# Kernel tuning notes

Hardware: AMD Instinct MI355X
Metric: run time of the kernel (lower is better)

Reference implementation:

```python
import jax, jax.numpy as jnp
import numpy as np

KROT = 8
DIM = 4096
GROUP = 128
N = 16384  # tokens (batch*seq)


def setup_inputs() -> dict:
    key = jax.random.key(0)
    k1, k2, k3 = jax.random.split(key, 3)
    x = jax.random.normal(k1, (N, DIM), dtype=jnp.float16)
    theta = (jax.random.normal(k2, (KROT, DIM // 2)) * 0.5).astype(jnp.float16)
    # pairs: per rotation layer, a permutation of [0, GROUP) tiled across groups
    # (matches torch.randperm(group_size).repeat(num_groups) in the module).
    rng = np.random.default_rng(0)
    single = np.stack([rng.permutation(GROUP) for _ in range(KROT)]).astype(np.int32)  # (KROT, GROUP)
    pairs = jnp.asarray(np.tile(single, (1, DIM // GROUP)))  # (KROT, DIM)
    channel_scales = jax.random.uniform(k3, (1, DIM), minval=0.5, maxval=1.5).astype(jnp.float16)
    return {"x": x, "pairs": pairs, "theta": theta,
            "channel_scales": channel_scales, "group_size": GROUP}


def reference(x, pairs, theta, channel_scales, group_size):
    """Pairwise Givens rotations + per-channel scaling.

    For each rotation layer k, channels are grouped into blocks of
    `group_size`; consecutive entries (pairs[k, 2i], pairs[k, 2i+1]) within a
    group define a rotated channel pair with angle theta[k, i].
    """
    krot, dim = pairs.shape
    # global channel index = group offset + within-group index from `pairs`
    offs = (jnp.arange(dim) // group_size) * group_size            # (dim,)
    gidx = pairs + offs[None, :]                                   # (krot, dim)
    a_idx = gidx[:, 0::2]                                          # (krot, dim//2)
    b_idx = gidx[:, 1::2]                                          # (krot, dim//2)

    for k in range(krot):  # krot is a small fixed constant (8)
        t = theta[k].astype(jnp.float32)
        c = jnp.cos(t).astype(x.dtype)                             # (dim//2,)
        s = jnp.sin(t).astype(x.dtype)
        xa = x[:, a_idx[k]]                                        # (N, dim//2)
        xb = x[:, b_idx[k]]
        x = x.at[:, a_idx[k]].set(c * xa - s * xb)
        x = x.at[:, b_idx[k]].set(s * xa + c * xb)
    return x * channel_scales
```

## Files before the change

### kernel.cpp

```cpp
#include <hip/hip_runtime.h>
#include <hip/hip_fp16.h>


typedef unsigned int uint32;
typedef unsigned short ushort;

#define DIM    4096
#define GROUP  128
#define KROT   8
#define NGROUP 32
#define TPAD   (GROUP + 1)

typedef float    f32x4 __attribute__((ext_vector_type(4)));
typedef _Float16 f16x8 __attribute__((ext_vector_type(8)));
typedef short    s16x8 __attribute__((ext_vector_type(8)));

__device__ __forceinline__ float bf16_to_f(ushort u) {
    union { uint32 i; float f; } v; v.i = ((uint32)u) << 16; return v.f;
}
__device__ __forceinline__ ushort f_to_bf16(float f) {
    union { float f; uint32 i; } v; v.f = f;
    uint32 x = v.i;
    return (ushort)((x + 0x7fffu + ((x >> 16) & 1u)) >> 16);
}
__device__ __forceinline__ float fp16_to_f(ushort u) {
    __half h = __ushort_as_half(u); return __half2float(h);
}
__device__ __forceinline__ ushort f_to_fp16(float f) {
    return __half_as_ushort(__float2half_rn(f));
}
__device__ __forceinline__ float bcast_f(float x, int lane) {
    return __uint_as_float(__builtin_amdgcn_readlane(__float_as_uint(x), lane));
}

__global__ __launch_bounds__(256) void detect_dtype(const uint32* __restrict__ scw,
                                                    int* __restrict__ flag) {
    __shared__ int cbf[256], cfp16[256];
    int b = 0, h = 0;
    for (int i = threadIdx.x; i < 2048; i += 256) {
        uint32 lo = scw[i] & 0xffffu;
        b += (lo >= 0x3F00u && lo <= 0x3FC0u);
        h += (lo >= 0x3800u && lo <= 0x3E00u);
    }
    cbf[threadIdx.x] = b; cfp16[threadIdx.x] = h;
    __syncthreads();
    for (int s = 128; s > 0; s >>= 1) {
        if (threadIdx.x < s) { cbf[threadIdx.x] += cbf[threadIdx.x + s];
                               cfp16[threadIdx.x] += cfp16[threadIdx.x + s]; }
        __syncthreads();
    }
    if (threadIdx.x == 0)
        *flag = (cbf[0] > 1024) ? 1 : ((cfp16[0] > 1024) ? 2 : 0);
}

__global__ __launch_bounds__(256) void compose_M(
    const int*  __restrict__ pairs,
    const void* __restrict__ thetav,
    const void* __restrict__ scalesv,
    ushort*     __restrict__ Mt,
    const int*  __restrict__ flagp)
{
    __shared__ float tile[64][TPAD];
    const int dt = *flagp;
    if (dt == 0) return;
    const int g    = blockIdx.x >> 1;
    const int half = blockIdx.x & 1;
    const int r0   = half * 64;
    const int tid  = threadIdx.x;
    const int l    = tid & 63;
    const int w    = tid >> 6;
    const int pmine = w * 16 + (l & 15);

    int A[KROT], B[KROT]; float C[KROT], S[KROT];
    #pragma unroll
    for (int k = 0; k < KROT; ++k) {
        A[k] = pairs[k * DIM + g * GROUP + 2 * pmine];
        B[k] = pairs[k * DIM + g * GROUP + 2 * pmine + 1];
        int ti = k * (DIM / 2) + g * (GROUP / 2) + pmine;
        float th = (dt == 1) ? bf16_to_f(((const ushort*)thetav)[ti])
                             : fp16_to_f(((const ushort*)thetav)[ti]);
        float c = __builtin_cosf(th), s = __builtin_sinf(th);
        if (dt == 1) { c = bf16_to_f(f_to_bf16(c)); s = bf16_to_f(f_to_bf16(s)); }
        else         { c = fp16_to_f(f_to_fp16(c)); s = fp16_to_f(f_to_fp16(s)); }
        C[k] = c; S[k] = s;
    }

    for (int idx = tid; idx < 64 * GROUP; idx += 256) {
        int r = idx >> 7, c = idx & 127;
        tile[r][c] = (r0 + r == c) ? 1.0f : 0.0f;
    }
    __syncthreads();

    #pragma unroll
    for (int k = 0; k < KROT; ++k) {
        #pragma unroll
        for (int pp = 0; pp < 16; ++pp) {
            int   a = __builtin_amdgcn_readlane(A[k], pp);
            int   b = __builtin_amdgcn_readlane(B[k], pp);
            float c = bcast_f(C[k], pp);
            float s = bcast_f(S[k], pp);
            float xa = tile[l][a], xb = tile[l][b];
            tile[l][a] = c * xa - s * xb;
            tile[l][b] = s * xa + c * xb;
        }
        __syncthreads();
    }

    for (int it = 0; it < 4; ++it) {
        int idx = it * 256 + tid;
        int j = idx >> 3, cc = idx & 7;
        float sj = (dt == 1) ? bf16_to_f(((const ushort*)scalesv)[g * GROUP + j])
                             : fp16_to_f(((const ushort*)scalesv)[g * GROUP + j]);
        uint32 ws4[4];
        #pragma unroll
        for (int h2 = 0; h2 < 4; ++h2) {
            float lo = tile[cc * 8 + 2 * h2][j]     * sj;
            float hi = tile[cc * 8 + 2 * h2 + 1][j] * sj;
            ushort ulo = (dt == 1) ? f_to_bf16(lo) : f_to_fp16(lo);
            ushort uhi = (dt == 1) ? f_to_bf16(hi) : f_to_fp16(hi);
            ws4[h2] = (uint32)ulo | ((uint32)uhi << 16);
        }
        uint4 v; v.x = ws4[0]; v.y = ws4[1]; v.z = ws4[2]; v.w = ws4[3];
        *(uint4*)(Mt + (size_t)g * GROUP * GROUP + (size_t)j * GROUP
                     + ((size_t)(half * 8 + cc)) * 8) = v;
    }
}

template <int DT>
__device__ __forceinline__ void gemm_core(const ushort* __restrict__ xs,
                                          const ushort* __restrict__ mt,
                                          f32x4 acc[2][4], int l, int wr, int wc)
{
    const int lr = l & 15, q = l >> 4;
    union U { uint4 u; f16x8 h; s16x8 s; };
    #pragma unroll
    for (int kk = 0; kk < 4; ++kk) {
        U av[2];
        #pragma unroll
        for (int mf = 0; mf < 2; ++mf) {
            int r = wr * 32 + mf * 16 + lr;
            int c = (kk * 4 + q) ^ (r & 7);
            av[mf].u = *(const uint4*)(xs + (size_t)r * GROUP + (size_t)c * 8);
        }
        #pragma unroll
        for (int nf = 0; nf < 4; ++nf) {
            int n = wc * 64 + nf * 16 + lr;
            int c = (kk * 4 + q) ^ (n & 7);
            U bv; bv.u = *(const uint4*)(mt + (size_t)n * GROUP + (size_t)c * 8);
            #pragma unroll
            for (int mf = 0; mf < 2; ++mf) {
                if constexpr (DT == 2)
                    acc[mf][nf] = __builtin_amdgcn_mfma_f32_16x16x32_f16(
                        av[mf].h, bv.h, acc[mf][nf], 0, 0, 0);
                else
                    acc[mf][nf] = __builtin_amdgcn_mfma_f32_16x16x32_bf16(
                        av[mf].s, bv.s, acc[mf][nf], 0, 0, 0);
            }
        }
    }
}

__global__ __launch_bounds__(256) void rotate_gemm(
    const void* __restrict__ Xv,
    const ushort* __restrict__ Mt,
    void* __restrict__ Outv,
    const int* __restrict__ flagp,
    const int* __restrict__ pairs,
    const void* __restrict__ thetav,
    const void* __restrict__ scalesv)
{
    __shared__ union __align__(16) {
        struct { ushort xs[64 * GROUP]; ushort mt[GROUP * GROUP]; } s;
        ushort os[64][136];
        struct { float tile[64][TPAD]; float scl[GROUP]; } fb;
    } sh;
    const int dt   = *flagp;
    const int row0 = blockIdx.x * 64;
    const int g    = blockIdx.y;
    const int tid  = threadIdx.x;
    const int l    = tid & 63;
    const int w    = tid >> 6;

    if (dt != 0) {
        const uint4* X4 = (const uint4*)Xv;
        #pragma unroll
        for (int it = 0; it < 4; ++it) {
            int i = it * 256 + tid;
            int r = i >> 4, c = i & 15;
            uint4 v = X4[(size_t)(row0 + r) * (DIM / 8) + g * (GROUP / 8) + c];
            *(uint4*)(sh.s.xs + (size_t)r * GROUP + (size_t)(c ^ (r & 7)) * 8) = v;
        }
        const uint4* M4 = (const uint4*)(Mt + (size_t)g * GROUP * GROUP);
        #pragma unroll
        for (int it = 0; it < 8; ++it) {
            int i = it * 256 + tid;
            int n = i >> 4, c = i & 15;
            uint4 v = M4[i];
            *(uint4*)(sh.s.mt + (size_t)n * GROUP + (size_t)(c ^ (n & 7)) * 8) = v;
        }
        __syncthreads();

        const int wr = w >> 1, wc = w & 1;
        f32x4 acc[2][4];
        #pragma unroll
        for (int mf = 0; mf < 2; ++mf)
            #pragma unroll
            for (int nf = 0; nf < 4; ++nf)
                acc[mf][nf] = (f32x4)0.0f;

        if (dt == 2) gemm_core<2>(sh.s.xs, sh.s.mt, acc, l, wr, wc);
        else         gemm_core<1>(sh.s.xs, sh.s.mt, acc, l, wr, wc);
        __syncthreads();

        const int lr = l & 15, q = l >> 4;
        #pragma unroll
        for (int mf = 0; mf < 2; ++mf) {
            #pragma unroll
            for (int nf = 0; nf < 4; ++nf) {
                int r  = wr * 32 + mf * 16 + q * 4;
                int cc = wc * 64 + nf * 16 + lr;
                #pragma unroll
                for (int j = 0; j < 4; ++j) {
                    float vv = acc[mf][nf][j];
                    sh.os[r + j][cc] = (dt == 1) ? f_to_bf16(vv) : f_to_fp16(vv);
                }
            }
        }
        __syncthreads();

        uint4* O4 = (uint4*)Outv;
        #pragma unroll
        for (int it = 0; it < 2; ++it) {
            int i = it * 256 + tid;
            int r = i >> 3, c8 = i & 7;
            uint4 v = *(const uint4*)(&sh.os[r][c8 * 8]);
            O4[(size_t)(row0 + r) * (DIM / 8) + g * (GROUP / 8) + c8] = v;
        }
        return;
    }

    const int pmine = w * 16 + (l & 15);
    if (tid < GROUP) sh.fb.scl[tid] = ((const float*)scalesv)[g * GROUP + tid];
    int A[KROT], B[KROT]; float C[KROT], S[KROT];
    #pragma unroll
    for (int k = 0; k < KROT; ++k) {
        A[k] = pairs[k * DIM + g * GROUP + 2 * pmine];
        B[k] = pairs[k * DIM + g * GROUP + 2 * pmine + 1];
        int ti = k * (DIM / 2) + g * (GROUP / 2) + pmine;
        float th = ((const float*)thetav)[ti];
        C[k] = __builtin_cosf(th); S[k] = __builtin_sinf(th);
    }
    const float4* Xf = (const float4*)Xv;
    for (int i = tid; i < 64 * 32; i += 256) {
        int r = i >> 5, c4 = i & 31;
        float4 v = Xf[(size_t)(row0 + r) * (DIM / 4) + g * (GROUP / 4) + c4];
        sh.fb.tile[r][c4 * 4 + 0] = v.x; sh.fb.tile[r][c4 * 4 + 1] = v.y;
        sh.fb.tile[r][c4 * 4 + 2] = v.z; sh.fb.tile[r][c4 * 4 + 3] = v.w;
    }
    __syncthreads();
    #pragma unroll
    for (int k = 0; k < KROT; ++k) {
        #pragma unroll
        for (int pp = 0; pp < 16; ++pp) {
            int   a = __builtin_amdgcn_readlane(A[k], pp);
            int   b = __builtin_amdgcn_readlane(B[k], pp);
            float c = bcast_f(C[k], pp);
            float s = bcast_f(S[k], pp);
            float xa = sh.fb.tile[l][a], xb = sh.fb.tile[l][b];
            sh.fb.tile[l][a] = c * xa - s * xb;
            sh.fb.tile[l][b] = s * xa + c * xb;
        }
        __syncthreads();
    }
    float4* Of = (float4*)Outv;
    for (int i = tid; i < 64 * 32; i += 256) {
        int r = i >> 5, c4 = i & 31;
        float4 v;
        v.x = sh.fb.tile[r][c4 * 4 + 0] * sh.fb.scl[c4 * 4 + 0];
        v.y = sh.fb.tile[r][c4 * 4 + 1] * sh.fb.scl[c4 * 4 + 1];
        v.z = sh.fb.tile[r][c4 * 4 + 2] * sh.fb.scl[c4 * 4 + 2];
        v.w = sh.fb.tile[r][c4 * 4 + 3] * sh.fb.scl[c4 * 4 + 3];
        Of[(size_t)(row0 + r) * (DIM / 4) + g * (GROUP / 4) + c4] = v;
    }
}

__global__ __launch_bounds__(256) void rotate_direct(
    const void* __restrict__ Xv,
    const int*  __restrict__ pairs,
    const void* __restrict__ thetav,
    const void* __restrict__ scalesv,
    void* __restrict__ Outv,
    const int* __restrict__ flagp, int defflag)
{
    __shared__ float tile[64][TPAD];
    __shared__ float scl[GROUP];
    const int g    = blockIdx.x;
    const int row0 = blockIdx.y * 64;
    const int tid  = threadIdx.x;
    const int dt   = flagp ? *flagp : defflag;
    const int l    = tid & 63;
    const int w    = tid >> 6;
    const int pmine = w * 16 + (l & 15);

    if (tid < GROUP) {
        int c = g * GROUP + tid;
        scl[tid] = (dt == 1) ? bf16_to_f(((const ushort*)scalesv)[c])
                 : (dt == 2) ? fp16_to_f(((const ushort*)scalesv)[c])
                 : ((const float*)scalesv)[c];
    }
    int A[KROT], B[KROT]; float C[KROT], S[KROT];
    #pragma unroll
    for (int k = 0; k < KROT; ++k) {
        A[k] = pairs[k * DIM + g * GROUP + 2 * pmine];
        B[k] = pairs[k * DIM + g * GROUP + 2 * pmine + 1];
        int ti = k * (DIM / 2) + g * (GROUP / 2) + pmine;
        float th = (dt == 1) ? bf16_to_f(((const ushort*)thetav)[ti])
                 : (dt == 2) ? fp16_to_f(((const ushort*)thetav)[ti])
                 : ((const float*)thetav)[ti];
        C[k] = __builtin_cosf(th);
        S[k] = __builtin_sinf(th);
    }
    if (dt == 0) {
        const float4* X4 = (const float4*)Xv;
        for (int i = tid; i < 64 * 32; i += 256) {
            int r = i >> 5, c4 = i & 31;
            float4 v = X4[(size_t)(row0 + r) * (DIM / 4) + g * (GROUP / 4) + c4];
            tile[r][c4 * 4 + 0] = v.x; tile[r][c4 * 4 + 1] = v.y;
            tile[r][c4 * 4 + 2] = v.z; tile[r][c4 * 4 + 3] = v.w;
        }
    } else {
        const uint4* X4 = (const uint4*)Xv;
        for (int i = tid; i < 64 * 16; i += 256) {
            int r = i >> 4, c8 = i & 15;
            uint4 wv = X4[(size_t)(row0 + r) * (DIM / 8) + g * (GROUP / 8) + c8];
            uint32 ws[4] = { wv.x, wv.y, wv.z, wv.w };
            #pragma unroll
            for (int h2 = 0; h2 < 4; ++h2) {
                ushort lo = (ushort)(ws[h2] & 0xffffu);
                ushort hi = (ushort)(ws[h2] >> 16);
                tile[r][c8 * 8 + 2 * h2]     = (dt == 1) ? bf16_to_f(lo) : fp16_to_f(lo);
                tile[r][c8 * 8 + 2 * h2 + 1] = (dt == 1) ? bf16_to_f(hi) : fp16_to_f(hi);
            }
        }
    }
    __syncthreads();
    #pragma unroll
    for (int k = 0; k < KROT; ++k) {
        #pragma unroll
        for (int pp = 0; pp < 16; ++pp) {
            int   a = __builtin_amdgcn_readlane(A[k], pp);
            int   b = __builtin_amdgcn_readlane(B[k], pp);
            float c = bcast_f(C[k], pp);
            float s = bcast_f(S[k], pp);
            float xa = tile[l][a], xb = tile[l][b];
            tile[l][a] = c * xa - s * xb;
            tile[l][b] = s * xa + c * xb;
        }
        __syncthreads();
    }
    if (dt == 0) {
        float4* O4 = (float4*)Outv;
        for (int i = tid; i < 64 * 32; i += 256) {
            int r = i >> 5, c4 = i & 31;
            float4 v;
            v.x = tile[r][c4 * 4 + 0] * scl[c4 * 4 + 0];
            v.y = tile[r][c4 * 4 + 1] * scl[c4 * 4 + 1];
            v.z = tile[r][c4 * 4 + 2] * scl[c4 * 4 + 2];
            v.w = tile[r][c4 * 4 + 3] * scl[c4 * 4 + 3];
            O4[(size_t)(row0 + r) * (DIM / 4) + g * (GROUP / 4) + c4] = v;
        }
    } else {
        uint4* O4 = (uint4*)Outv;
        for (int i = tid; i < 64 * 16; i += 256) {
            int r = i >> 4, c8 = i & 15;
            uint32 ws[4];
            #pragma unroll
            for (int h2 = 0; h2 < 4; ++h2) {
                float lo = tile[r][c8 * 8 + 2 * h2]     * scl[c8 * 8 + 2 * h2];
                float hi = tile[r][c8 * 8 + 2 * h2 + 1] * scl[c8 * 8 + 2 * h2 + 1];
                ushort ulo = (dt == 1) ? f_to_bf16(lo) : f_to_fp16(lo);
                ushort uhi = (dt == 1) ? f_to_bf16(hi) : f_to_fp16(hi);
                ws[h2] = (uint32)ulo | ((uint32)uhi << 16);
            }
            uint4 wv; wv.x = ws[0]; wv.y = ws[1]; wv.z = ws[2]; wv.w = ws[3];
            O4[(size_t)(row0 + r) * (DIM / 8) + g * (GROUP / 8) + c8] = wv;
        }
    }
}

extern "C" void kernel_launch(void* const* d_in, const int* in_sizes, int n_in,
                              void* d_out, int out_size, void* d_ws, size_t ws_size,
                              hipStream_t stream) {
    const void* x      = d_in[0];
    const int*  pairs  = (const int*)d_in[1];
    const void* theta  = d_in[2];
    const void* scales = d_in[3];

    const int N16 = in_sizes[0] / DIM;
    const int nrowtiles = N16 / 64;

    const size_t NEED = 64 + (size_t)NGROUP * GROUP * GROUP * 2;

    if (d_ws != nullptr && ws_size >= NEED) {
        int*    flag = (int*)d_ws;
        ushort* Mt   = (ushort*)((char*)d_ws + 64);
        detect_dtype<<<1, 256, 0, stream>>>((const uint32*)scales, flag);
        compose_M<<<64, 256, 0, stream>>>(pairs, theta, scales, Mt, flag);
        rotate_gemm<<<dim3(nrowtiles, NGROUP), 256, 0, stream>>>(
            x, Mt, d_out, flag, pairs, theta, scales);
    } else if (d_ws != nullptr && ws_size >= sizeof(int)) {
        int* flag = (int*)d_ws;
        detect_dtype<<<1, 256, 0, stream>>>((const uint32*)scales, flag);
        rotate_direct<<<dim3(NGROUP, nrowtiles), 256, 0, stream>>>(
            x, pairs, theta, scales, d_out, flag, 0);
    } else {
        rotate_direct<<<dim3(NGROUP, nrowtiles), 256, 0, stream>>>(
            x, pairs, theta, scales, d_out, nullptr, 0);
    }
}
```

Baseline: 525.2 us.

## Move composed-matrix MFMA path to fp32 inputs using split-fp16 hi/lo products

Result: faster. 472.7 us (-10.0%).

```diff
diff --git a/kernel.cpp b/kernel.cpp
--- a/kernel.cpp
+++ b/kernel.cpp
@@ -13,7 +13,8 @@
 
 typedef float    f32x4 __attribute__((ext_vector_type(4)));
 typedef _Float16 f16x8 __attribute__((ext_vector_type(8)));
-typedef short    s16x8 __attribute__((ext_vector_type(8)));
+
+union Uh { uint4 u; f16x8 h; };
 
 __device__ __forceinline__ float bf16_to_f(ushort u) {
     union { uint32 i; float f; } v; v.i = ((uint32)u) << 16; return v.f;
@@ -31,6 +32,9 @@
 }
 __device__ __forceinline__ float bcast_f(float x, int lane) {
     return __uint_as_float(__builtin_amdgcn_readlane(__float_as_uint(x), lane));
+}
+__device__ __forceinline__ ushort h_bits(_Float16 h) {
+    union { _Float16 f; ushort s; } v; v.f = h; return v.s;
 }
 
 __global__ __launch_bounds__(256) void detect_dtype(const uint32* __restrict__ scw,
@@ -57,12 +61,13 @@
     const int*  __restrict__ pairs,
     const void* __restrict__ thetav,
     const void* __restrict__ scalesv,
-    ushort*     __restrict__ Mt,
+    ushort*     __restrict__ Mth,
+    ushort*     __restrict__ Mtl,
     const int*  __restrict__ flagp)
 {
     __shared__ float tile[64][TPAD];
     const int dt = *flagp;
-    if (dt == 0) return;
+    if (dt != 0) return;
     const int g    = blockIdx.x >> 1;
     const int half = blockIdx.x & 1;
     const int r0   = half * 64;
@@ -71,216 +76,250 @@
     const int w    = tid >> 6;
     const int pmine = w * 16 + (l & 15);
 
-    int A[KROT], B[KROT]; float C[KROT], S[KROT];
+    int Ak[KROT], Bk[KROT]; float Ck[KROT], Sk[KROT];
     #pragma unroll
     for (int k = 0; k < KROT; ++k) {
-        A[k] = pairs[k * DIM + g * GROUP + 2 * pmine];
-        B[k] = pairs[k * DIM + g * GROUP + 2 * pmine + 1];
-        int ti = k * (DIM / 2) + g * (GROUP / 2) + pmine;
-        float th = (dt == 1) ? bf16_to_f(((const ushort*)thetav)[ti])
-                             : fp16_to_f(((const ushort*)thetav)[ti]);
-        float c = __builtin_cosf(th), s = __builtin_sinf(th);
-        if (dt == 1) { c = bf16_to_f(f_to_bf16(c)); s = bf16_to_f(f_to_bf16(s)); }
-        else         { c = fp16_to_f(f_to_fp16(c)); s = fp16_to_f(f_to_fp16(s)); }
-        C[k] = c; S[k] = s;
-    }
-
+        Ak[k] = pairs[k * DIM + g * GROUP + 2 * pmine];
+        Bk[k] = pairs[k * DIM + g * GROUP + 2 * pmine + 1];
+        float th = ((const float*)thetav)[k * (DIM / 2) + g * (GROUP / 2) + pmine];
+        Ck[k] = __builtin_cosf(th); Sk[k] = __builtin_sinf(th);
+    }
     for (int idx = tid; idx < 64 * GROUP; idx += 256) {
         int r = idx >> 7, c = idx & 127;
         tile[r][c] = (r0 + r == c) ? 1.0f : 0.0f;
-    }
-    __syncthreads();
-
-    #pragma unroll
-    for (int k = 0; k < KROT; ++k) {
-        #pragma unroll
-        for (int pp = 0; pp < 16; ++pp) {
-            int   a = __builtin_amdgcn_readlane(A[k], pp);
-            int   b = __builtin_amdgcn_readlane(B[k], pp);
-            float c = bcast_f(C[k], pp);
-            float s = bcast_f(S[k], pp);
-            float xa = tile[l][a], xb = tile[l][b];
-            tile[l][a] = c * xa - s * xb;
-            tile[l][b] = s * xa + c * xb;
-        }
-        __syncthreads();
-    }
-
-    for (int it = 0; it < 4; ++it) {
-        int idx = it * 256 + tid;
-        int j = idx >> 3, cc = idx & 7;
-        float sj = (dt == 1) ? bf16_to_f(((const ushort*)scalesv)[g * GROUP + j])
-                             : fp16_to_f(((const ushort*)scalesv)[g * GROUP + j]);
-        uint32 ws4[4];
-        #pragma unroll
-        for (int h2 = 0; h2 < 4; ++h2) {
-            float lo = tile[cc * 8 + 2 * h2][j]     * sj;
-            float hi = tile[cc * 8 + 2 * h2 + 1][j] * sj;
-            ushort ulo = (dt == 1) ? f_to_bf16(lo) : f_to_fp16(lo);
-            ushort uhi = (dt == 1) ? f_to_bf16(hi) : f_to_fp16(hi);
-            ws4[h2] = (uint32)ulo | ((uint32)uhi << 16);
-        }
-        uint4 v; v.x = ws4[0]; v.y = ws4[1]; v.z = ws4[2]; v.w = ws4[3];
-        *(uint4*)(Mt + (size_t)g * GROUP * GROUP + (size_t)j * GROUP
-                     + ((size_t)(half * 8 + cc)) * 8) = v;
-    }
-}
-
-template <int DT>
-__device__ __forceinline__ void gemm_core(const ushort* __restrict__ xs,
-                                          const ushort* __restrict__ mt,
-                                          f32x4 acc[2][4], int l, int wr, int wc)
-{
-    const int lr = l & 15, q = l >> 4;
-    union U { uint4 u; f16x8 h; s16x8 s; };
-    #pragma unroll
-    for (int kk = 0; kk < 4; ++kk) {
-        U av[2];
-        #pragma unroll
-        for (int mf = 0; mf < 2; ++mf) {
-            int r = wr * 32 + mf * 16 + lr;
-            int c = (kk * 4 + q) ^ (r & 7);
-            av[mf].u = *(const uint4*)(xs + (size_t)r * GROUP + (size_t)c * 8);
-        }
-        #pragma unroll
-        for (int nf = 0; nf < 4; ++nf) {
-            int n = wc * 64 + nf * 16 + lr;
-            int c = (kk * 4 + q) ^ (n & 7);
-            U bv; bv.u = *(const uint4*)(mt + (size_t)n * GROUP + (size_t)c * 8);
-            #pragma unroll
-            for (int mf = 0; mf < 2; ++mf) {
-                if constexpr (DT == 2)
-                    acc[mf][nf] = __builtin_amdgcn_mfma_f32_16x16x32_f16(
-                        av[mf].h, bv.h, acc[mf][nf], 0, 0, 0);
-                else
-                    acc[mf][nf] = __builtin_amdgcn_mfma_f32_16x16x32_bf16(
-                        av[mf].s, bv.s, acc[mf][nf], 0, 0, 0);
-            }
-        }
-    }
-}
-
-__global__ __launch_bounds__(256) void rotate_gemm(
-    const void* __restrict__ Xv,
-    const ushort* __restrict__ Mt,
-    void* __restrict__ Outv,
-    const int* __restrict__ flagp,
-    const int* __restrict__ pairs,
-    const void* __restrict__ thetav,
-    const void* __restrict__ scalesv)
-{
-    __shared__ union __align__(16) {
-        struct { ushort xs[64 * GROUP]; ushort mt[GROUP * GROUP]; } s;
-        ushort os[64][136];
-        struct { float tile[64][TPAD]; float scl[GROUP]; } fb;
-    } sh;
-    const int dt   = *flagp;
-    const int row0 = blockIdx.x * 64;
-    const int g    = blockIdx.y;
-    const int tid  = threadIdx.x;
-    const int l    = tid & 63;
-    const int w    = tid >> 6;
-
-    if (dt != 0) {
-        const uint4* X4 = (const uint4*)Xv;
-        #pragma unroll
-        for (int it = 0; it < 4; ++it) {
-            int i = it * 256 + tid;
-            int r = i >> 4, c = i & 15;
-            uint4 v = X4[(size_t)(row0 + r) * (DIM / 8) + g * (GROUP / 8) + c];
-            *(uint4*)(sh.s.xs + (size_t)r * GROUP + (size_t)(c ^ (r & 7)) * 8) = v;
-        }
-        const uint4* M4 = (const uint4*)(Mt + (size_t)g * GROUP * GROUP);
-        #pragma unroll
-        for (int it = 0; it < 8; ++it) {
-            int i = it * 256 + tid;
-            int n = i >> 4, c = i & 15;
-            uint4 v = M4[i];
-            *(uint4*)(sh.s.mt + (size_t)n * GROUP + (size_t)(c ^ (n & 7)) * 8) = v;
-        }
-        __syncthreads();
-
-        const int wr = w >> 1, wc = w & 1;
-        f32x4 acc[2][4];
-        #pragma unroll
-        for (int mf = 0; mf < 2; ++mf)
-            #pragma unroll
-            for (int nf = 0; nf < 4; ++nf)
-                acc[mf][nf] = (f32x4)0.0f;
-
-        if (dt == 2) gemm_core<2>(sh.s.xs, sh.s.mt, acc, l, wr, wc);
-        else         gemm_core<1>(sh.s.xs, sh.s.mt, acc, l, wr, wc);
-        __syncthreads();
-
-        const int lr = l & 15, q = l >> 4;
-        #pragma unroll
-        for (int mf = 0; mf < 2; ++mf) {
-            #pragma unroll
-            for (int nf = 0; nf < 4; ++nf) {
-                int r  = wr * 32 + mf * 16 + q * 4;
-                int cc = wc * 64 + nf * 16 + lr;
-                #pragma unroll
-                for (int j = 0; j < 4; ++j) {
-                    float vv = acc[mf][nf][j];
-                    sh.os[r + j][cc] = (dt == 1) ? f_to_bf16(vv) : f_to_fp16(vv);
-                }
-            }
-        }
-        __syncthreads();
-
-        uint4* O4 = (uint4*)Outv;
-        #pragma unroll
-        for (int it = 0; it < 2; ++it) {
-            int i = it * 256 + tid;
-            int r = i >> 3, c8 = i & 7;
-            uint4 v = *(const uint4*)(&sh.os[r][c8 * 8]);
-            O4[(size_t)(row0 + r) * (DIM / 8) + g * (GROUP / 8) + c8] = v;
-        }
-        return;
-    }
-
-    const int pmine = w * 16 + (l & 15);
-    if (tid < GROUP) sh.fb.scl[tid] = ((const float*)scalesv)[g * GROUP + tid];
-    int A[KROT], B[KROT]; float C[KROT], S[KROT];
-    #pragma unroll
-    for (int k = 0; k < KROT; ++k) {
-        A[k] = pairs[k * DIM + g * GROUP + 2 * pmine];
-        B[k] = pairs[k * DIM + g * GROUP + 2 * pmine + 1];
-        int ti = k * (DIM / 2) + g * (GROUP / 2) + pmine;
-        float th = ((const float*)thetav)[ti];
-        C[k] = __builtin_cosf(th); S[k] = __builtin_sinf(th);
-    }
-    const float4* Xf = (const float4*)Xv;
-    for (int i = tid; i < 64 * 32; i += 256) {
-        int r = i >> 5, c4 = i & 31;
-        float4 v = Xf[(size_t)(row0 + r) * (DIM / 4) + g * (GROUP / 4) + c4];
-        sh.fb.tile[r][c4 * 4 + 0] = v.x; sh.fb.tile[r][c4 * 4 + 1] = v.y;
-        sh.fb.tile[r][c4 * 4 + 2] = v.z; sh.fb.tile[r][c4 * 4 + 3] = v.w;
     }
     __syncthreads();
     #pragma unroll
     for (int k = 0; k < KROT; ++k) {
         #pragma unroll
         for (int pp = 0; pp < 16; ++pp) {
-            int   a = __builtin_amdgcn_readlane(A[k], pp);
-            int   b = __builtin_amdgcn_readlane(B[k], pp);
-            float c = bcast_f(C[k], pp);
-            float s = bcast_f(S[k], pp);
-            float xa = sh.fb.tile[l][a], xb = sh.fb.tile[l][b];
-            sh.fb.tile[l][a] = c * xa - s * xb;
-            sh.fb.tile[l][b] = s * xa + c * xb;
+            int   a = __builtin_amdgcn_readlane(Ak[k], pp);
+            int   b = __builtin_amdgcn_readlane(Bk[k], pp);
+            float c = bcast_f(Ck[k], pp);
+            float s = bcast_f(Sk[k], pp);
+            float xa = tile[l][a], xb = tile[l][b];
+            tile[l][a] = c * xa - s * xb;
+            tile[l][b] = s * xa + c * xb;
         }
         __syncthreads();
     }
-    float4* Of = (float4*)Outv;
-    for (int i = tid; i < 64 * 32; i += 256) {
-        int r = i >> 5, c4 = i & 31;
-        float4 v;
-        v.x = sh.fb.tile[r][c4 * 4 + 0] * sh.fb.scl[c4 * 4 + 0];
-        v.y = sh.fb.tile[r][c4 * 4 + 1] * sh.fb.scl[c4 * 4 + 1];
-        v.z = sh.fb.tile[r][c4 * 4 + 2] * sh.fb.scl[c4 * 4 + 2];
-        v.w = sh.fb.tile[r][c4 * 4 + 3] * sh.fb.scl[c4 * 4 + 3];
-        Of[(size_t)(row0 + r) * (DIM / 4) + g * (GROUP / 4) + c4] = v;
+    for (int it = 0; it < 4; ++it) {
+        int idx = it * 256 + tid;
+        int j = idx >> 3, cc = idx & 7;
+        float sj = ((const float*)scalesv)[g * GROUP + j];
+        union { ushort s[8]; uint4 u; } ph, pl;
+        #pragma unroll
+        for (int e = 0; e < 8; ++e) {
+            float m = tile[cc * 8 + e][j] * sj;
+            _Float16 hh = (_Float16)m;
+            float r = m - (float)hh;
+            ph.s[e] = h_bits(hh);
+            pl.s[e] = h_bits((_Float16)r);
+        }
+        size_t off = (size_t)g * (GROUP * GROUP) + (size_t)j * GROUP + r0 + cc * 8;
+        *(uint4*)(Mth + off) = ph.u;
+        *(uint4*)(Mtl + off) = pl.u;
+    }
+}
+
+__global__ __launch_bounds__(256, 1) void rotate_gemm(
+    const void* __restrict__ Xv,
+    const ushort* __restrict__ Mth,
+    const ushort* __restrict__ Mtl,
+    void* __restrict__ Outv,
+    const int* __restrict__ flagp,
+    const int* __restrict__ pairs,
+    const void* __restrict__ thetav,
+    const void* __restrict__ scalesv,
+    int nrows)
+{
+    __shared__ float tile[64][TPAD];
+    __shared__ float scl[GROUP];
+    const int dt  = *flagp;
+    const int bid = blockIdx.x;
+    const int g   = bid & 31;
+    const int sub = bid >> 5;
+    const int ntiles = nrows >> 6;
+    const int tid = threadIdx.x;
+    const int l   = tid & 63;
+    const int w   = tid >> 6;
+    const int lr  = l & 15;
+    const int q   = l >> 4;
+
+    if (dt == 0) {
+        const int wr = w >> 1, wc = w & 1;
+        const float* Xg = (const float*)Xv;
+        float*       Og = (float*)Outv;
+
+        uint4 BH[4][4], BL[4][4];
+        #pragma unroll
+        for (int nf = 0; nf < 4; ++nf) {
+            #pragma unroll
+            for (int kk = 0; kk < 4; ++kk) {
+                size_t off = (size_t)g * (GROUP * GROUP)
+                           + (size_t)(wc * 64 + nf * 16 + lr) * GROUP
+                           + kk * 32 + q * 8;
+                BH[nf][kk] = *(const uint4*)(Mth + off);
+                BL[nf][kk] = *(const uint4*)(Mtl + off);
+            }
+        }
+
+        uint4 A0[2][4][2], A1[2][4][2];
+
+        auto loadA = [&](uint4 (&A)[2][4][2], int t) {
+            const int R0 = t * 64;
+            #pragma unroll
+            for (int mf = 0; mf < 2; ++mf) {
+                #pragma unroll
+                for (int kk = 0; kk < 4; ++kk) {
+                    const float* p = Xg + (size_t)(R0 + wr * 32 + mf * 16 + lr) * DIM
+                                        + g * GROUP + kk * 32 + q * 8;
+                    A[mf][kk][0] = *(const uint4*)p;
+                    A[mf][kk][1] = *(const uint4*)(p + 4);
+                }
+            }
+        };
+
+        auto computeStore = [&](const uint4 (&A)[2][4][2], int t) {
+            f16x8 ah[2][4], al[2][4];
+            #pragma unroll
+            for (int mf = 0; mf < 2; ++mf) {
+                #pragma unroll
+                for (int kk = 0; kk < 4; ++kk) {
+                    f16x8 hv, lv;
+                    #pragma unroll
+                    for (int h4 = 0; h4 < 2; ++h4) {
+                        union { uint4 u; float f[4]; } uu; uu.u = A[mf][kk][h4];
+                        #pragma unroll
+                        for (int e = 0; e < 4; ++e) {
+                            float x = uu.f[e];
+                            _Float16 hh = (_Float16)x;
+                            float r = x - (float)hh;
+                            hv[h4 * 4 + e] = hh;
+                            lv[h4 * 4 + e] = (_Float16)r;
+                        }
+                    }
+                    ah[mf][kk] = hv; al[mf][kk] = lv;
+                }
+            }
+            f32x4 acc[2][4];
+            #pragma unroll
+            for (int mf = 0; mf < 2; ++mf)
+                #pragma unroll
+                for (int nf = 0; nf < 4; ++nf)
+                    acc[mf][nf] = (f32x4)0.0f;
+            #pragma unroll
+            for (int kk = 0; kk < 4; ++kk) {
+                #pragma unroll
+                for (int nf = 0; nf < 4; ++nf) {
+                    Uh bh, bl; bh.u = BH[nf][kk]; bl.u = BL[nf][kk];
+                    #pragma unroll
+                    for (int mf = 0; mf < 2; ++mf) {
+                        acc[mf][nf] = __builtin_amdgcn_mfma_f32_16x16x32_f16(
+                            ah[mf][kk], bh.h, acc[mf][nf], 0, 0, 0);
+                        acc[mf][nf] = __builtin_amdgcn_mfma_f32_16x16x32_f16(
+                            al[mf][kk], bh.h, acc[mf][nf], 0, 0, 0);
+                        acc[mf][nf] = __builtin_amdgcn_mfma_f32_16x16x32_f16(
+                            ah[mf][kk], bl.h, acc[mf][nf], 0, 0, 0);
+                    }
+                }
+            }
+            const int R0 = t * 64;
+            #pragma unroll
+            for (int mf = 0; mf < 2; ++mf) {
+                #pragma unroll
+                for (int nf = 0; nf < 4; ++nf) {
+                    float* bp = Og + (size_t)(R0 + wr * 32 + mf * 16 + q * 4) * DIM
+                                   + g * GROUP + wc * 64 + nf * 16 + lr;
+                    #pragma unroll
+                    for (int j = 0; j < 4; ++j)
+                        __builtin_nontemporal_store(acc[mf][nf][j], bp + (size_t)j * DIM);
+                }
+            }
+        };
+
+        int t = sub;
+        if (t < ntiles) {
+            loadA(A0, t);
+            while (true) {
+                int t1 = t + 8;
+                if (t1 < ntiles) loadA(A1, t1);
+                computeStore(A0, t);
+                if (t1 >= ntiles) break;
+                int t2 = t1 + 8;
+                if (t2 < ntiles) loadA(A0, t2);
+                computeStore(A1, t1);
+                if (t2 >= ntiles) break;
+                t = t2;
+            }
+        }
+        return;
+    }
+
+    {
+        const int pmine = w * 16 + (l & 15);
+        if (tid < GROUP) {
+            int c = g * GROUP + tid;
+            scl[tid] = (dt == 1) ? bf16_to_f(((const ushort*)scalesv)[c])
+                                 : fp16_to_f(((const ushort*)scalesv)[c]);
+        }
+        int Ak[KROT], Bk[KROT]; float Ck[KROT], Sk[KROT];
+        #pragma unroll
+        for (int k = 0; k < KROT; ++k) {
+            Ak[k] = pairs[k * DIM + g * GROUP + 2 * pmine];
+            Bk[k] = pairs[k * DIM + g * GROUP + 2 * pmine + 1];
+            int ti = k * (DIM / 2) + g * (GROUP / 2) + pmine;
+            float th = (dt == 1) ? bf16_to_f(((const ushort*)thetav)[ti])
+                                 : fp16_to_f(((const ushort*)thetav)[ti]);
+            Ck[k] = __builtin_cosf(th); Sk[k] = __builtin_sinf(th);
+        }
+        for (int t = sub; t < ntiles; t += 8) {
+            const int row0 = t * 64;
+            const uint4* X4 = (const uint4*)Xv;
+            for (int i = tid; i < 64 * 16; i += 256) {
+                int r = i >> 4, c8 = i & 15;
+                uint4 wv = X4[(size_t)(row0 + r) * (DIM / 8) + g * (GROUP / 8) + c8];
+                uint32 ws[4] = { wv.x, wv.y, wv.z, wv.w };
+                #pragma unroll
+                for (int h2 = 0; h2 < 4; ++h2) {
+                    ushort lo = (ushort)(ws[h2] & 0xffffu);
+                    ushort hi = (ushort)(ws[h2] >> 16);
+                    tile[r][c8 * 8 + 2 * h2]     = (dt == 1) ? bf16_to_f(lo) : fp16_to_f(lo);
+                    tile[r][c8 * 8 + 2 * h2 + 1] = (dt == 1) ? bf16_to_f(hi) : fp16_to_f(hi);
+                }
+            }
+            __syncthreads();
+            #pragma unroll
+            for (int k = 0; k < KROT; ++k) {
+                #pragma unroll
+                for (int pp = 0; pp < 16; ++pp) {
+                    int   a = __builtin_amdgcn_readlane(Ak[k], pp);
+                    int   b = __builtin_amdgcn_readlane(Bk[k], pp);
+                    float c = bcast_f(Ck[k], pp);
+                    float s = bcast_f(Sk[k], pp);
+                    float xa = tile[l][a], xb = tile[l][b];
+                    tile[l][a] = c * xa - s * xb;
+                    tile[l][b] = s * xa + c * xb;
+                }
+                __syncthreads();
+            }
+            uint4* O4 = (uint4*)Outv;
+            for (int i = tid; i < 64 * 16; i += 256) {
+                int r = i >> 4, c8 = i & 15;
+                uint32 ws[4];
+                #pragma unroll
+                for (int h2 = 0; h2 < 4; ++h2) {
+                    float lo = tile[r][c8 * 8 + 2 * h2]     * scl[c8 * 8 + 2 * h2];
+                    float hi = tile[r][c8 * 8 + 2 * h2 + 1] * scl[c8 * 8 + 2 * h2 + 1];
+                    ushort ulo = (dt == 1) ? f_to_bf16(lo) : f_to_fp16(lo);
+                    ushort uhi = (dt == 1) ? f_to_bf16(hi) : f_to_fp16(hi);
+                    ws[h2] = (uint32)ulo | ((uint32)uhi << 16);
+                }
+                uint4 wv; wv.x = ws[0]; wv.y = ws[1]; wv.z = ws[2]; wv.w = ws[3];
+                O4[(size_t)(row0 + r) * (DIM / 8) + g * (GROUP / 8) + c8] = wv;
+            }
+            __syncthreads();
+        }
     }
 }
 
@@ -308,17 +347,17 @@
                  : (dt == 2) ? fp16_to_f(((const ushort*)scalesv)[c])
                  : ((const float*)scalesv)[c];
     }
-    int A[KROT], B[KROT]; float C[KROT], S[KROT];
+    int Ak[KROT], Bk[KROT]; float Ck[KROT], Sk[KROT];
     #pragma unroll
     for (int k = 0; k < KROT; ++k) {
-        A[k] = pairs[k * DIM + g * GROUP + 2 * pmine];
-        B[k] = pairs[k * DIM + g * GROUP + 2 * pmine + 1];
+        Ak[k] = pairs[k * DIM + g * GROUP + 2 * pmine];
+        Bk[k] = pairs[k * DIM + g * GROUP + 2 * pmine + 1];
         int ti = k * (DIM / 2) + g * (GROUP / 2) + pmine;
         float th = (dt == 1) ? bf16_to_f(((const ushort*)thetav)[ti])
                  : (dt == 2) ? fp16_to_f(((const ushort*)thetav)[ti])
                  : ((const float*)thetav)[ti];
-        C[k] = __builtin_cosf(th);
-        S[k] = __builtin_sinf(th);
+        Ck[k] = __builtin_cosf(th);
+        Sk[k] = __builtin_sinf(th);
     }
     if (dt == 0) {
         const float4* X4 = (const float4*)Xv;
@@ -348,10 +387,10 @@
     for (int k = 0; k < KROT; ++k) {
         #pragma unroll
         for (int pp = 0; pp < 16; ++pp) {
-            int   a = __builtin_amdgcn_readlane(A[k], pp);
-            int   b = __builtin_amdgcn_readlane(B[k], pp);
-            float c = bcast_f(C[k], pp);
-            float s = bcast_f(S[k], pp);
+            int   a = __builtin_amdgcn_readlane(Ak[k], pp);
+            int   b = __builtin_amdgcn_readlane(Bk[k], pp);
+            float c = bcast_f(Ck[k], pp);
+            float s = bcast_f(Sk[k], pp);
             float xa = tile[l][a], xb = tile[l][b];
             tile[l][a] = c * xa - s * xb;
             tile[l][b] = s * xa + c * xb;
@@ -396,18 +435,20 @@
     const void* theta  = d_in[2];
     const void* scales = d_in[3];
 
-    const int N16 = in_sizes[0] / DIM;
-    const int nrowtiles = N16 / 64;
-
-    const size_t NEED = 64 + (size_t)NGROUP * GROUP * GROUP * 2;
+    const int nrows = in_sizes[0] / DIM;
+    const int nrowtiles = nrows / 64;
+
+    const size_t MSZ  = (size_t)NGROUP * GROUP * GROUP * 2;
+    const size_t NEED = 64 + 2 * MSZ;
 
     if (d_ws != nullptr && ws_size >= NEED) {
         int*    flag = (int*)d_ws;
-        ushort* Mt   = (ushort*)((char*)d_ws + 64);
+        ushort* Mth  = (ushort*)((char*)d_ws + 64);
+        ushort* Mtl  = (ushort*)((char*)d_ws + 64 + MSZ);
         detect_dtype<<<1, 256, 0, stream>>>((const uint32*)scales, flag);
-        compose_M<<<64, 256, 0, stream>>>(pairs, theta, scales, Mt, flag);
-        rotate_gemm<<<dim3(nrowtiles, NGROUP), 256, 0, stream>>>(
-            x, Mt, d_out, flag, pairs, theta, scales);
+        compose_M<<<64, 256, 0, stream>>>(pairs, theta, scales, Mth, Mtl, flag);
+        rotate_gemm<<<256, 256, 0, stream>>>(
+            x, Mth, Mtl, d_out, flag, pairs, theta, scales, nrows);
     } else if (d_ws != nullptr && ws_size >= sizeof(int)) {
         int* flag = (int*)d_ws;
         detect_dtype<<<1, 256, 0, stream>>>((const uint32*)scales, flag);
```
